# Optimization experiments

Measured on AMD Instinct MI355X. Metric: run time of the kernel, lower is better.

## Reference

```python
import jax, jax.numpy as jnp
import numpy as np
from jax import lax

NUM_KP = 17
MAX_PEOPLE = 30
HEAT_THRESH = 0.1
STRIDE = 4  # heatmap -> image coordinate scale

def setup_inputs() -> dict:
    key = jax.random.key(0)
    heatmaps = jax.random.uniform(key, (32, NUM_KP, 256, 256), dtype=jnp.float32)
    return {"heatmaps": heatmaps}

def reference(heatmaps):
    # heatmaps: [B, C, H, W]
    B, C, H, W = heatmaps.shape
    neg_inf = jnp.float32(-jnp.inf)
    # 3x3 max-pool NMS (stride 1, pad 1) batched over all B*C channels at once.
    hmax = lax.reduce_window(
        heatmaps, neg_inf, lax.max,
        window_dimensions=(1, 1, 3, 3),
        window_strides=(1, 1, 1, 1),
        padding=((0, 0), (0, 0), (1, 1), (1, 1)),
    )
    nms = heatmaps * (hmax == heatmaps).astype(heatmaps.dtype)
    # Threshold + descending sort + take top max_people, done as a batched top_k.
    flat = nms.reshape(B, C, H * W)
    masked = jnp.where(flat > HEAT_THRESH, flat, neg_inf)
    scores, idx = lax.top_k(masked, MAX_PEOPLE)          # [B, C, max_people]
    y = idx // W
    x = idx % W
    coords = jnp.stack([x, y], axis=-1).astype(jnp.int32) * STRIDE  # [B,C,max_people,2] as (x,y)*4
    valid = scores > HEAT_THRESH                          # padding mask (original output is ragged)
    return coords, scores, valid
```

## Files before the change

kernel.cpp:

```cpp
#include <hip/hip_runtime.h>
#include <stdint.h>

#define NUM_KP 17
#define BATCH  32
#define HDIM   256
#define WDIM   256
#define NCH    (BATCH * NUM_KP)
#define MAXP   30
#define THREADS 512
#define NWAVES  8
#define SEGCAP  1280

#define NBINS  4096
#define QB     125953

__device__ __forceinline__ unsigned long long shfl_down_u64(unsigned long long v, int off) {
    unsigned lo = (unsigned)v, hi = (unsigned)(v >> 32);
    lo = __shfl_down(lo, off);
    hi = __shfl_down(hi, off);
    return ((unsigned long long)hi << 32) | lo;
}
__device__ __forceinline__ unsigned long long shfl_u64(unsigned long long v, int lane) {
    unsigned lo = (unsigned)v, hi = (unsigned)(v >> 32);
    lo = __shfl(lo, lane);
    hi = __shfl(hi, lane);
    return ((unsigned long long)hi << 32) | lo;
}
__device__ __forceinline__ unsigned quant12(float v) {
    int b = (int)(__float_as_uint(v) >> 13) - QB;
    b = b < 1 ? 1 : (b > NBINS - 1 ? NBINS - 1 : b);
    return (unsigned)b;
}

__global__ __launch_bounds__(THREADS, 6)
void pose_fused_kernel(const float* __restrict__ heat, float* __restrict__ out, int out_size) {
    __shared__ unsigned s_buf[NWAVES * SEGCAP];
    __shared__ unsigned s_hist[NBINS / 2];
    __shared__ int s_gsum[256];
    __shared__ unsigned long long s_ref[256];
    __shared__ int s_wcnt[NWAVES];
    __shared__ int s_nref, s_tau;

    const int tid  = threadIdx.x;
    const int chan = blockIdx.x;
    const int wave = tid >> 6;
    const int lane = tid & 63;
    const float NEGINF = -__builtin_inff();
    const float* __restrict__ cp = heat + (size_t)chan * (HDIM * WDIM);

    for (int i = tid; i < NBINS / 2; i += THREADS) s_hist[i] = 0;
    if (tid == 0) s_nref = 0;
    __syncthreads();

    const int r0 = wave << 5;
    const float* colp = cp + (lane << 2);
    const float4 NEG4 = make_float4(NEGINF, NEGINF, NEGINF, NEGINF);
    const unsigned long long ltmask = (1ull << lane) - 1ull;
    unsigned* __restrict__ seg = s_buf + wave * SEGCAP;
    int wavecnt = 0;

    auto LD = [&](int r) -> float4 {
        return (r >= 0 && r < HDIM) ? *(const float4*)(colp + (r << 8)) : NEG4;
    };
    auto push = [&](float v, int pidx, int pos) {
        if (pos < SEGCAP) {
            unsigned q = quant12(v);
            seg[pos] = (q << 16) | (unsigned)pidx;
            atomicAdd(&s_hist[q >> 1], 1u << ((q & 1) << 4));
        }
    };
    auto process = [&](const float4& up, const float4& md, const float4& dn, int r) {
        float vm0 = fmaxf(up.x, fmaxf(md.x, dn.x));
        float vm1 = fmaxf(up.y, fmaxf(md.y, dn.y));
        float vm2 = fmaxf(up.z, fmaxf(md.z, dn.z));
        float vm3 = fmaxf(up.w, fmaxf(md.w, dn.w));
        float left  = __shfl_up(vm3, 1);   if (lane == 0)  left  = NEGINF;
        float right = __shfl_down(vm0, 1); if (lane == 63) right = NEGINF;
        float h0 = fmaxf(left, fmaxf(vm0, vm1));
        float h1 = fmaxf(vm0, fmaxf(vm1, vm2));
        float h2 = fmaxf(vm1, fmaxf(vm2, vm3));
        float h3 = fmaxf(vm2, fmaxf(vm3, right));

        bool p0 = md.x > 0.1f && md.x == h0;
        bool p1 = md.y > 0.1f && md.y == h1;
        bool p2 = md.z > 0.1f && md.z == h2;
        bool p3 = md.w > 0.1f && md.w == h3;
        unsigned long long b0 = __ballot(p0), b1 = __ballot(p1);
        unsigned long long b2 = __ballot(p2), b3 = __ballot(p3);
        int c0 = __popcll(b0), c1 = __popcll(b1), c2 = __popcll(b2);
        int before = wavecnt;
        wavecnt += c0 + c1 + c2 + __popcll(b3);

        const int base = (r << 8) | (lane << 2);
        if (p0) push(md.x, base + 0, before + __popcll(b0 & ltmask));
        if (p1) push(md.y, base + 1, before + c0 + __popcll(b1 & ltmask));
        if (p2) push(md.z, base + 2, before + c0 + c1 + __popcll(b2 & ltmask));
        if (p3) push(md.w, base + 3, before + c0 + c1 + c2 + __popcll(b3 & ltmask));
    };

    float4 rm   = LD(r0 - 1);
    float4 cur0 = LD(r0 + 0), cur1 = LD(r0 + 1), cur2 = LD(r0 + 2), cur3 = LD(r0 + 3);
    #pragma unroll
    for (int g = 0; g < 8; ++g) {
        const int rb = r0 + (g << 2);
        float4 n0, n1, n2, n3;
        if (g < 7) { n0 = LD(rb + 4); n1 = LD(rb + 5); n2 = LD(rb + 6); n3 = LD(rb + 7); }
        else       { n0 = LD(rb + 4); n1 = NEG4; n2 = NEG4; n3 = NEG4; }
        process(rm,   cur0, cur1, rb + 0);
        process(cur0, cur1, cur2, rb + 1);
        process(cur1, cur2, cur3, rb + 2);
        process(cur2, cur3, n0,   rb + 3);
        rm = cur3; cur0 = n0; cur1 = n1; cur2 = n2; cur3 = n3;
    }
    if (lane == 0) s_wcnt[wave] = wavecnt < SEGCAP ? wavecnt : SEGCAP;
    __syncthreads();

    if (tid < 256) {
        int s = 0;
        #pragma unroll
        for (int j = 0; j < 8; ++j) {
            unsigned w = s_hist[tid * 8 + j];
            s += (int)(w & 0xFFFFu) + (int)(w >> 16);
        }
        s_gsum[tid] = s;
    }
    __syncthreads();
    if (wave == 0) {
        int u0 = s_gsum[(lane << 2) + 0], u1 = s_gsum[(lane << 2) + 1];
        int u2 = s_gsum[(lane << 2) + 2], u3 = s_gsum[(lane << 2) + 3];
        int t = u0 + u1 + u2 + u3;
        int R = t;
        #pragma unroll
        for (int off = 1; off < 64; off <<= 1) {
            int v = __shfl_down(R, off);
            if (lane + off < 64) R += v;
        }
        int E = R - t;
        int sg3 = u3 + E, sg2 = u2 + sg3, sg1 = u1 + sg2, sg0 = u0 + sg1;
        unsigned long long mask = __ballot(sg0 >= MAXP);
        if (mask == 0ull) {
            if (lane == 0) s_tau = 0;
        } else {
            int hi = 63 - __builtin_clzll(mask);
            if (lane == hi) {
                int k, above;
                if      (sg3 >= MAXP) { k = 3; above = E;   }
                else if (sg2 >= MAXP) { k = 2; above = sg3; }
                else if (sg1 >= MAXP) { k = 1; above = sg2; }
                else                  { k = 0; above = sg1; }
                int g = (lane << 2) + k;
                int cum = above, tau = 0;
                for (int b = (g << 4) + 15; b >= (g << 4); --b) {
                    cum += (int)((s_hist[b >> 1] >> ((b & 1) << 4)) & 0xFFFFu);
                    if (cum >= MAXP) { tau = b; break; }
                }
                s_tau = tau;
            }
        }
    }
    __syncthreads();

    const unsigned tau = (unsigned)s_tau;
    for (int s = 0; s < NWAVES; ++s) {
        const int c = s_wcnt[s];
        const unsigned* sb = s_buf + s * SEGCAP;
        for (int i = tid; i < c; i += THREADS) {
            unsigned p = sb[i];
            if ((p >> 16) >= tau) {
                int pos = atomicAdd(&s_nref, 1);
                if (pos < 256) {
                    unsigned idx = p & 0xFFFFu;
                    float sc = cp[idx];
                    s_ref[pos] = ((unsigned long long)__float_as_uint(sc) << 32) | (unsigned)(~idx);
                }
            }
        }
    }
    __syncthreads();
    const int nref = s_nref < 256 ? s_nref : 256;

    if (tid < 64) {
        unsigned long long k0 = (tid       < nref) ? s_ref[tid]       : 0ull;
        unsigned long long k1 = (tid + 64  < nref) ? s_ref[tid + 64]  : 0ull;
        unsigned long long k2 = (tid + 128 < nref) ? s_ref[tid + 128] : 0ull;
        unsigned long long k3 = (tid + 192 < nref) ? s_ref[tid + 192] : 0ull;
        for (int r = 0; r < MAXP; ++r) {
            unsigned long long best = k0; int bs = 0;
            if (k1 > best) { best = k1; bs = 1; }
            if (k2 > best) { best = k2; bs = 2; }
            if (k3 > best) { best = k3; bs = 3; }
            unsigned long long key = best;
            int slot = (bs << 6) | tid;
            #pragma unroll
            for (int off = 32; off > 0; off >>= 1) {
                unsigned long long ok = shfl_down_u64(key, off);
                int os = __shfl_down(slot, off);
                if (ok > key) { key = ok; slot = os; }
            }
            key  = shfl_u64(key, 0);
            slot = __shfl(slot, 0);
            if ((slot & 63) == tid) {
                int which = slot >> 6;
                if      (which == 0) k0 = 0ull;
                else if (which == 1) k1 = 0ull;
                else if (which == 2) k2 = 0ull;
                else                 k3 = 0ull;
            }
            if (tid == 0) {
                float sc, vld; unsigned idx;
                if (key != 0ull) {
                    sc  = __uint_as_float((unsigned)(key >> 32));
                    idx = (~(unsigned)key) & 0xFFFFu;
                    vld = 1.0f;
                } else { sc = NEGINF; idx = 0u; vld = 0.0f; }
                int x = (int)(idx & 255), y = (int)(idx >> 8);
                long long cb = ((long long)chan * MAXP + r) * 2;
                if (cb + 1 < out_size) {
                    out[cb]     = (float)(x * 4);
                    out[cb + 1] = (float)(y * 4);
                }
                long long so = (long long)NCH * MAXP * 2 + (long long)chan * MAXP + r;
                if (so < out_size) out[so] = sc;
                long long vo = (long long)NCH * MAXP * 3 + (long long)chan * MAXP + r;
                if (vo < out_size) out[vo] = vld;
            }
        }
    }
}

extern "C" void kernel_launch(void* const* d_in, const int* in_sizes, int n_in,
                              void* d_out, int out_size, void* d_ws, size_t ws_size,
                              hipStream_t stream) {
    const float* heat = (const float*)d_in[0];
    float* out = (float*)d_out;
    hipLaunchKernelGGL(pose_fused_kernel, dim3(NCH), dim3(THREADS), 0, stream, heat, out, out_size);
}
```

Baseline: 238.4 us.

## Split each channel across four blocks with a second merge kernel

Each channel's 256x256 heatmap is now handled by four 256-thread blocks, one per quarter of the rows. Each block runs NMS, its own histogram threshold and a local top-30, and writes packed keys to workspace. A small 64-thread merge kernel then picks the global top-30 per channel and writes the outputs. The aim is more blocks, smaller per-block shared memory and higher occupancy. The cost is a second launch, redundant histogram and selection work per quarter, and halo rows reloaded at quarter boundaries.

```diff
diff --git a/kernel.cpp b/kernel.cpp
--- a/kernel.cpp
+++ b/kernel.cpp
@@ -7,12 +7,14 @@
 #define WDIM   256
 #define NCH    (BATCH * NUM_KP)
 #define MAXP   30
-#define THREADS 512
-#define NWAVES  8
-#define SEGCAP  1280
+#define QBLKS  4
+#define K1THREADS 256
+#define SEGCAP 640
 
 #define NBINS  4096
 #define QB     125953
+
+#define WS_REQUIRED ((size_t)NCH * QBLKS * MAXP * 8)
 
 __device__ __forceinline__ unsigned long long shfl_down_u64(unsigned long long v, int off) {
     unsigned lo = (unsigned)v, hi = (unsigned)(v >> 32);
@@ -32,27 +34,28 @@
     return (unsigned)b;
 }
 
-__global__ __launch_bounds__(THREADS, 6)
-void pose_fused_kernel(const float* __restrict__ heat, float* __restrict__ out, int out_size) {
-    __shared__ unsigned s_buf[NWAVES * SEGCAP];
+__global__ __launch_bounds__(K1THREADS, 7)
+void pose_part_kernel(const float* __restrict__ heat, unsigned long long* __restrict__ part) {
+    __shared__ unsigned s_buf[4 * SEGCAP];
     __shared__ unsigned s_hist[NBINS / 2];
     __shared__ int s_gsum[256];
     __shared__ unsigned long long s_ref[256];
-    __shared__ int s_wcnt[NWAVES];
+    __shared__ int s_wcnt[4];
     __shared__ int s_nref, s_tau;
 
     const int tid  = threadIdx.x;
-    const int chan = blockIdx.x;
+    const int chan = blockIdx.x >> 2;
+    const int qtr  = blockIdx.x & 3;
     const int wave = tid >> 6;
     const int lane = tid & 63;
     const float NEGINF = -__builtin_inff();
     const float* __restrict__ cp = heat + (size_t)chan * (HDIM * WDIM);
 
-    for (int i = tid; i < NBINS / 2; i += THREADS) s_hist[i] = 0;
+    for (int i = tid; i < NBINS / 2; i += K1THREADS) s_hist[i] = 0;
     if (tid == 0) s_nref = 0;
     __syncthreads();
 
-    const int r0 = wave << 5;
+    const int r0 = (qtr << 6) + (wave << 4);
     const float* colp = cp + (lane << 2);
     const float4 NEG4 = make_float4(NEGINF, NEGINF, NEGINF, NEGINF);
     const unsigned long long ltmask = (1ull << lane) - 1ull;
@@ -101,10 +104,10 @@
     float4 rm   = LD(r0 - 1);
     float4 cur0 = LD(r0 + 0), cur1 = LD(r0 + 1), cur2 = LD(r0 + 2), cur3 = LD(r0 + 3);
     #pragma unroll
-    for (int g = 0; g < 8; ++g) {
+    for (int g = 0; g < 4; ++g) {
         const int rb = r0 + (g << 2);
         float4 n0, n1, n2, n3;
-        if (g < 7) { n0 = LD(rb + 4); n1 = LD(rb + 5); n2 = LD(rb + 6); n3 = LD(rb + 7); }
+        if (g < 3) { n0 = LD(rb + 4); n1 = LD(rb + 5); n2 = LD(rb + 6); n3 = LD(rb + 7); }
         else       { n0 = LD(rb + 4); n1 = NEG4; n2 = NEG4; n3 = NEG4; }
         process(rm,   cur0, cur1, rb + 0);
         process(cur0, cur1, cur2, rb + 1);
@@ -115,7 +118,7 @@
     if (lane == 0) s_wcnt[wave] = wavecnt < SEGCAP ? wavecnt : SEGCAP;
     __syncthreads();
 
-    if (tid < 256) {
+    {
         int s = 0;
         #pragma unroll
         for (int j = 0; j < 8; ++j) {
@@ -161,10 +164,10 @@
     __syncthreads();
 
     const unsigned tau = (unsigned)s_tau;
-    for (int s = 0; s < NWAVES; ++s) {
+    for (int s = 0; s < 4; ++s) {
         const int c = s_wcnt[s];
         const unsigned* sb = s_buf + s * SEGCAP;
-        for (int i = tid; i < c; i += THREADS) {
+        for (int i = tid; i < c; i += K1THREADS) {
             unsigned p = sb[i];
             if ((p >> 16) >= tau) {
                 int pos = atomicAdd(&s_nref, 1);
@@ -180,6 +183,7 @@
     const int nref = s_nref < 256 ? s_nref : 256;
 
     if (tid < 64) {
+        unsigned long long* pk = part + (size_t)blockIdx.x * MAXP;
         unsigned long long k0 = (tid       < nref) ? s_ref[tid]       : 0ull;
         unsigned long long k1 = (tid + 64  < nref) ? s_ref[tid + 64]  : 0ull;
         unsigned long long k2 = (tid + 128 < nref) ? s_ref[tid + 128] : 0ull;
@@ -206,24 +210,55 @@
                 else if (which == 2) k2 = 0ull;
                 else                 k3 = 0ull;
             }
-            if (tid == 0) {
-                float sc, vld; unsigned idx;
-                if (key != 0ull) {
-                    sc  = __uint_as_float((unsigned)(key >> 32));
-                    idx = (~(unsigned)key) & 0xFFFFu;
-                    vld = 1.0f;
-                } else { sc = NEGINF; idx = 0u; vld = 0.0f; }
-                int x = (int)(idx & 255), y = (int)(idx >> 8);
-                long long cb = ((long long)chan * MAXP + r) * 2;
-                if (cb + 1 < out_size) {
-                    out[cb]     = (float)(x * 4);
-                    out[cb + 1] = (float)(y * 4);
-                }
-                long long so = (long long)NCH * MAXP * 2 + (long long)chan * MAXP + r;
-                if (so < out_size) out[so] = sc;
-                long long vo = (long long)NCH * MAXP * 3 + (long long)chan * MAXP + r;
-                if (vo < out_size) out[vo] = vld;
-            }
+            if (tid == 0) pk[r] = key;
+        }
+    }
+}
+
+__global__ __launch_bounds__(64)
+void pose_merge_kernel(const unsigned long long* __restrict__ part,
+                       float* __restrict__ out, int out_size) {
+    const int chan = blockIdx.x;
+    const int lane = threadIdx.x;
+    const float NEGINF = -__builtin_inff();
+    const unsigned long long* pk = part + (size_t)chan * (QBLKS * MAXP);
+
+    unsigned long long k0 = pk[lane];
+    unsigned long long k1 = (lane + 64 < QBLKS * MAXP) ? pk[lane + 64] : 0ull;
+
+    for (int r = 0; r < MAXP; ++r) {
+        unsigned long long best = k0; int bs = 0;
+        if (k1 > best) { best = k1; bs = 1; }
+        unsigned long long key = best;
+        int slot = (bs << 6) | lane;
+        #pragma unroll
+        for (int off = 32; off > 0; off >>= 1) {
+            unsigned long long ok = shfl_down_u64(key, off);
+            int os = __shfl_down(slot, off);
+            if (ok > key) { key = ok; slot = os; }
+        }
+        key  = shfl_u64(key, 0);
+        slot = __shfl(slot, 0);
+        if ((slot & 63) == lane) {
+            if ((slot >> 6) == 0) k0 = 0ull; else k1 = 0ull;
+        }
+        if (lane == 0) {
+            float sc, vld; unsigned idx;
+            if (key != 0ull) {
+                sc  = __uint_as_float((unsigned)(key >> 32));
+                idx = (~(unsigned)key) & 0xFFFFu;
+                vld = 1.0f;
+            } else { sc = NEGINF; idx = 0u; vld = 0.0f; }
+            int x = (int)(idx & 255), y = (int)(idx >> 8);
+            long long cb = ((long long)chan * MAXP + r) * 2;
+            if (cb + 1 < out_size) {
+                out[cb]     = (float)(x * 4);
+                out[cb + 1] = (float)(y * 4);
+            }
+            long long so = (long long)NCH * MAXP * 2 + (long long)chan * MAXP + r;
+            if (so < out_size) out[so] = sc;
+            long long vo = (long long)NCH * MAXP * 3 + (long long)chan * MAXP + r;
+            if (vo < out_size) out[vo] = vld;
         }
     }
 }
@@ -233,5 +268,9 @@
                               hipStream_t stream) {
     const float* heat = (const float*)d_in[0];
     float* out = (float*)d_out;
-    hipLaunchKernelGGL(pose_fused_kernel, dim3(NCH), dim3(THREADS), 0, stream, heat, out, out_size);
-}
+    unsigned long long* part = (unsigned long long*)d_ws;
+    hipLaunchKernelGGL(pose_part_kernel, dim3(NCH * QBLKS), dim3(K1THREADS), 0, stream,
+                       heat, part);
+    hipLaunchKernelGGL(pose_merge_kernel, dim3(NCH), dim3(64), 0, stream,
+                       part, out, out_size);
+}
```

Result: no change. 237.6 us (-0.3%).
